# Performance work log

Measured on AMD Instinct MI355X. Metric: run time of the kernel, lower is better.

## Reference

```python
import jax, jax.numpy as jnp
import numpy as np

B, C, H, W = 128, 3, 224, 224
NUM_CLASSES = 1000
MIN_CUT, MAX_CUT = 64, 160
BATCH_PROB = 0.1


def setup_inputs() -> dict:
    key = jax.random.key(0)
    k1, k2, k3, k4, k5, k6, k7 = jax.random.split(key, 7)
    images = jax.random.normal(k1, (B, C, H, W), dtype=jnp.float32)
    labels = jax.random.uniform(k2, (B, NUM_CLASSES), dtype=jnp.float32)
    perm = jax.random.permutation(k3, B).astype(jnp.int32)          # torch.randperm
    box_size = jax.random.randint(k4, (B,), MIN_CUT, MAX_CUT + 1).astype(jnp.int32)
    # x in [0, H - box_size], y in [0, W - box_size], per-sample valid corners
    ux = jax.random.uniform(k5, (B,))
    uy = jax.random.uniform(k6, (B,))
    x = jnp.floor(ux * (H - box_size + 1).astype(jnp.float32)).astype(jnp.int32)
    y = jnp.floor(uy * (W - box_size + 1).astype(jnp.float32)).astype(jnp.int32)
    keep = jax.random.uniform(k7, (B,)) > BATCH_PROB                # rand(1) > batch_prob
    return {"images": images, "labels": labels, "perm": perm,
            "box_size": box_size, "x": x, "y": y, "keep": keep}


def reference(images, labels, perm, box_size, x, y, keep):
    # shuffled pairs
    shuff_imgs = images[perm]           # [B,C,H,W]
    shuff_labels = labels[perm]         # [B,K]
    # vectorized per-sample box mask
    r = jnp.arange(H)                   # rows
    c = jnp.arange(W)                   # cols
    row_in = (r[None, :] >= x[:, None]) & (r[None, :] < (x + box_size)[:, None])   # [B,H]
    col_in = (c[None, :] >= y[:, None]) & (c[None, :] < (y + box_size)[:, None])   # [B,W]
    mask = row_in[:, :, None] & col_in[:, None, :]                                  # [B,H,W]
    mask = mask & keep[:, None, None]
    out_imgs = jnp.where(mask[:, None, :, :], shuff_imgs, images)                   # [B,C,H,W]
    # label mixing: lam = 1 - box^2/(H*W)
    lam = 1.0 - (box_size.astype(jnp.float32) ** 2) / float(H * W)                  # [B]
    mixed = lam[:, None] * labels + (1.0 - lam)[:, None] * shuff_labels
    out_labels = jnp.where(keep[:, None], mixed, labels)
    return out_imgs, out_labels
```

## Files before the change

kernel.cpp:

```cpp
#include <hip/hip_runtime.h>

#define BB 128
#define CC 3
#define HH 224
#define WW 224
#define KK 1000

#define WV (WW / 4)
#define PLANE (HH * WV)
#define PER_B (CC * PLANE)
#define IMG_BLOCKS (PER_B / 256)
#define KV (KK / 4)

typedef float v4f __attribute__((ext_vector_type(4)));

__global__ __launch_bounds__(256) void cutmix_fused_kernel(
        const float* __restrict__ img,
        const float* __restrict__ lab,
        const int* __restrict__ perm,
        const int* __restrict__ box,
        const int* __restrict__ xs,
        const int* __restrict__ ys,
        const int* __restrict__ keep,
        float* __restrict__ out_img,
        float* __restrict__ out_lab) {
    const int b = blockIdx.y;
    const int kp = keep[b];
    const int x0 = xs[b];
    const int bs = box[b];
    const int y0 = ys[b];
    const int pb = perm[b];

    if (blockIdx.x < IMG_BLOCKS) {
        int idx = blockIdx.x * 256 + threadIdx.x;
        int c  = idx / PLANE;
        int r  = idx - c * PLANE;
        int h  = r / WV;
        int wv = r - h * WV;
        int w0 = wv * 4;

        size_t base = (((size_t)(b * CC + c) * HH) + h) * WW + w0;
        v4f v;
        bool row_in = kp && ((unsigned)(h - x0) < (unsigned)bs);
        if (row_in) {
            int y1 = y0 + bs;
            bool full = (w0 >= y0) && (w0 + 4 <= y1);
            size_t sbase = (((size_t)(pb * CC + c) * HH) + h) * WW + w0;
            v = *reinterpret_cast<const v4f*>(img + (full ? sbase : base));
            if (!full && (w0 + 4 > y0) && (w0 < y1)) {
                v4f s = *reinterpret_cast<const v4f*>(img + sbase);
#pragma unroll
                for (int j = 0; j < 4; ++j) {
                    int w = w0 + j;
                    if (w >= y0 && w < y1) v[j] = s[j];
                }
            }
        } else {
            v = *reinterpret_cast<const v4f*>(img + base);
        }
        __builtin_nontemporal_store(v, reinterpret_cast<v4f*>(out_img + base));
    } else {
        int kv = threadIdx.x;
        if (kv >= KV) return;
        size_t base = (size_t)b * KK + kv * 4;
        v4f l = *reinterpret_cast<const v4f*>(lab + base);
        v4f o = l;
        if (kp) {
            float bsf = (float)bs;
            float lam = 1.0f - bsf * bsf / (float)(HH * WW);
            float om = 1.0f - lam;
            v4f s = *reinterpret_cast<const v4f*>(lab + (size_t)pb * KK + kv * 4);
            o = lam * l + om * s;
        }
        __builtin_nontemporal_store(o, reinterpret_cast<v4f*>(out_lab + base));
    }
}

extern "C" void kernel_launch(void* const* d_in, const int* in_sizes, int n_in,
                              void* d_out, int out_size, void* d_ws, size_t ws_size,
                              hipStream_t stream) {
    const float* images = (const float*)d_in[0];
    const float* labels = (const float*)d_in[1];
    const int* perm     = (const int*)d_in[2];
    const int* box      = (const int*)d_in[3];
    const int* xs       = (const int*)d_in[4];
    const int* ys       = (const int*)d_in[5];
    const int* keep     = (const int*)d_in[6];

    float* out_imgs = (float*)d_out;
    float* out_labs = (float*)d_out + (size_t)BB * CC * HH * WW;

    dim3 grid(IMG_BLOCKS + 1, BB);
    cutmix_fused_kernel<<<grid, 256, 0, stream>>>(
        images, labels, perm, box, xs, ys, keep, out_imgs, out_labs);
}
```

Baseline: 30.97 us.

## Process four vectors per thread and switch to regular stores

```diff
diff --git a/kernel.cpp b/kernel.cpp
--- a/kernel.cpp
+++ b/kernel.cpp
@@ -9,7 +9,8 @@
 #define WV (WW / 4)
 #define PLANE (HH * WV)
 #define PER_B (CC * PLANE)
-#define IMG_BLOCKS (PER_B / 256)
+#define VPT 4
+#define IMG_BLOCKS ((PER_B + 256 * VPT - 1) / (256 * VPT))
 #define KV (KK / 4)
 
 typedef float v4f __attribute__((ext_vector_type(4)));
@@ -32,33 +33,50 @@
     const int pb = perm[b];
 
     if (blockIdx.x < IMG_BLOCKS) {
-        int idx = blockIdx.x * 256 + threadIdx.x;
-        int c  = idx / PLANE;
-        int r  = idx - c * PLANE;
-        int h  = r / WV;
-        int wv = r - h * WV;
-        int w0 = wv * 4;
+        const int y1 = y0 + bs;
+        v4f v[VPT];
+        size_t base[VPT];
+        bool valid[VPT];
 
-        size_t base = (((size_t)(b * CC + c) * HH) + h) * WW + w0;
-        v4f v;
-        bool row_in = kp && ((unsigned)(h - x0) < (unsigned)bs);
-        if (row_in) {
-            int y1 = y0 + bs;
-            bool full = (w0 >= y0) && (w0 + 4 <= y1);
-            size_t sbase = (((size_t)(pb * CC + c) * HH) + h) * WW + w0;
-            v = *reinterpret_cast<const v4f*>(img + (full ? sbase : base));
-            if (!full && (w0 + 4 > y0) && (w0 < y1)) {
-                v4f s = *reinterpret_cast<const v4f*>(img + sbase);
 #pragma unroll
-                for (int j = 0; j < 4; ++j) {
-                    int w = w0 + j;
-                    if (w >= y0 && w < y1) v[j] = s[j];
+        for (int j = 0; j < VPT; ++j) {
+            int idx = blockIdx.x * (256 * VPT) + j * 256 + threadIdx.x;
+            valid[j] = idx < PER_B;
+            if (valid[j]) {
+                int c  = idx / PLANE;
+                int r  = idx - c * PLANE;
+                int h  = r / WV;
+                int wv = r - h * WV;
+                int w0 = wv * 4;
+
+                size_t ba = (((size_t)(b * CC + c) * HH) + h) * WW + w0;
+                base[j] = ba;
+                bool row_in = kp && ((unsigned)(h - x0) < (unsigned)bs);
+                bool full = false, eg = false;
+                size_t sbase = 0;
+                if (row_in) {
+                    full = (w0 >= y0) && (w0 + 4 <= y1);
+                    bool any = (w0 + 4 > y0) && (w0 < y1);
+                    eg = any && !full;
+                    sbase = (((size_t)(pb * CC + c) * HH) + h) * WW + w0;
+                }
+                v[j] = *reinterpret_cast<const v4f*>(img + (full ? sbase : ba));
+                if (eg) {
+                    v4f s = *reinterpret_cast<const v4f*>(img + sbase);
+#pragma unroll
+                    for (int q = 0; q < 4; ++q) {
+                        int w = w0 + q;
+                        if (w >= y0 && w < y1) v[j][q] = s[q];
+                    }
                 }
             }
-        } else {
-            v = *reinterpret_cast<const v4f*>(img + base);
         }
-        __builtin_nontemporal_store(v, reinterpret_cast<v4f*>(out_img + base));
+#pragma unroll
+        for (int j = 0; j < VPT; ++j) {
+            if (valid[j]) {
+                *reinterpret_cast<v4f*>(out_img + base[j]) = v[j];
+            }
+        }
     } else {
         int kv = threadIdx.x;
         if (kv >= KV) return;
@@ -72,7 +90,7 @@
             v4f s = *reinterpret_cast<const v4f*>(lab + (size_t)pb * KK + kv * 4);
             o = lam * l + om * s;
         }
-        __builtin_nontemporal_store(o, reinterpret_cast<v4f*>(out_lab + base));
+        *reinterpret_cast<v4f*>(out_lab + base) = o;
     }
 }
 
```

Result: faster. 30.34 us (-2.0%).
